# Optimization experiments

Measured on AMD Instinct MI355X. Metric: run time of the kernel, lower is better.

The kernel has to match this reference:

```python
import jax, jax.numpy as jnp
import numpy as np

RMS_EPS = 1.1920928955078125e-07  # torch.finfo(float32).eps, nn.RMSNorm default when eps=None


def setup_inputs() -> dict:
    key = jax.random.key(0)
    ks = jax.random.split(key, 7)
    B, T, C, Wh, E, K = 8, 4096, 256, 1024, 8, 2
    return {
        "x": jax.random.normal(ks[0], (B, T, C), dtype=jnp.float32),
        "rms_weight": jnp.ones((C,), dtype=jnp.float32),
        "W1": jax.random.normal(ks[1], (E, C, Wh), dtype=jnp.float32),
        "b1": jax.random.normal(ks[2], (E, Wh), dtype=jnp.float32),
        "W2": jax.random.normal(ks[3], (E, Wh, C), dtype=jnp.float32),
        "b2": jax.random.normal(ks[4], (E, C), dtype=jnp.float32),
        "expert_ids": jax.random.randint(ks[5], (B, T, K), 0, E, dtype=jnp.int64),
    }


def reference(x, rms_weight, W1, b1, W2, b2, expert_ids):
    # RMSNorm over last dim (torch nn.RMSNorm, eps = float32 eps)
    xn = x * jax.lax.rsqrt(jnp.mean(x * x, axis=-1, keepdims=True) + RMS_EPS) * rms_weight
    # Per-expert 2-layer MLP. The torch code gathers per-token weight copies then bmm's;
    # mathematically identical (and far cheaper in memory) is: run every expert densely,
    # then gather the K selected expert outputs per token.
    h = jax.nn.gelu(jnp.einsum("btc,ecw->btew", xn, W1) + b1, approximate=False)  # [B,T,E,Wh]
    y = jnp.einsum("btew,ewc->btec", h, W2) + b2  # [B,T,E,C]
    # gather selected experts: [B,T,K,C]; dropout p is 0.0 (eval) -> identity
    out = jnp.take_along_axis(y, expert_ids[..., None], axis=2)
    return out
```

## Files before the change

kernel.cpp:

```cpp
#include <hip/hip_runtime.h>
#include <cstdint>

typedef unsigned short ushort_t;
typedef __bf16 bf16x8 __attribute__((ext_vector_type(8)));
typedef ushort_t u16x8 __attribute__((ext_vector_type(8)));
typedef float f32x4 __attribute__((ext_vector_type(4)));
typedef uint32_t u32x4 __attribute__((ext_vector_type(4)));

#define RMS_EPS 1.1920928955078125e-07f

__device__ __forceinline__ ushort_t f2bf(float f) {
  uint32_t u = __builtin_bit_cast(uint32_t, f);
  u += 0x7fffu + ((u >> 16) & 1u);
  return (ushort_t)(u >> 16);
}

__device__ __forceinline__ void g2l16(const ushort_t* g, ushort_t* l) {
  __builtin_amdgcn_global_load_lds(
      (const __attribute__((address_space(1))) uint32_t*)g,
      (__attribute__((address_space(3))) uint32_t*)l, 16, 0, 0);
}

__global__ void rmsnorm_cast(const float* __restrict__ x, const float* __restrict__ w,
                             ushort_t* __restrict__ xn) {
  int token = blockIdx.x * 4 + (threadIdx.x >> 6);
  int lane = threadIdx.x & 63;
  const float4* row = reinterpret_cast<const float4*>(x + (size_t)token * 256);
  float4 v = row[lane];
  float s = v.x * v.x + v.y * v.y + v.z * v.z + v.w * v.w;
#pragma unroll
  for (int off = 1; off < 64; off <<= 1) s += __shfl_xor(s, off);
  float inv = rsqrtf(s * (1.0f / 256.0f) + RMS_EPS);
  const float4* wr = reinterpret_cast<const float4*>(w);
  float4 wv = wr[lane];
  ushort4 o;
  o.x = f2bf(v.x * inv * wv.x);
  o.y = f2bf(v.y * inv * wv.y);
  o.z = f2bf(v.z * inv * wv.z);
  o.w = f2bf(v.w * inv * wv.w);
  *reinterpret_cast<ushort4*>(xn + (size_t)token * 256 + lane * 4) = o;
}

__global__ __launch_bounds__(256) void pack_w(const float* __restrict__ W1,
                                              const float* __restrict__ W2,
                                              ushort_t* __restrict__ w1f,
                                              ushort_t* __restrict__ w2f) {
  __shared__ ushort_t tile[64][130];
  int b = blockIdx.x;
  int isW2 = b >= 256;
  const float* src; ushort_t* dst; int e, kt, wt, rs;
  if (!isW2) { e = b >> 5; kt = (b >> 3) & 3; wt = b & 7; src = W1; dst = w1f; rs = 1024; }
  else { b -= 256; e = b >> 5; kt = (b >> 1) & 15; wt = b & 1; src = W2; dst = w2f; rs = 256; }
  int k0 = kt * 64, c0 = wt * 128;
  const float* sb = src + ((size_t)e << 18) + (size_t)k0 * rs + c0;
  int t = threadIdx.x;
#pragma unroll
  for (int i = 0; i < 8; ++i) {
    int f = i * 1024 + t * 4;
    int r = f >> 7, c = f & 127;
    float4 v = *reinterpret_cast<const float4*>(sb + (size_t)r * rs + c);
    ushort2 lo, hi;
    lo.x = f2bf(v.x); lo.y = f2bf(v.y); hi.x = f2bf(v.z); hi.y = f2bf(v.w);
    *reinterpret_cast<ushort2*>(&tile[r][c]) = lo;
    *reinterpret_cast<ushort2*>(&tile[r][c + 2]) = hi;
  }
  __syncthreads();
  int lane = t & 63, l16 = lane & 15, quad = lane >> 4;
#pragma unroll
  for (int p = 0; p < 4; ++p) {
    int u = p * 256 + t;
    int kk2 = (u >> 9) & 1;
    int rr = kk2 * 32 + quad * 8;
    u16x8 o;
    size_t U;
    if (!isW2) {
      int nt = (u >> 6) & 1, chL = (u >> 7) & 3;
      int cc = chL * 32 + nt * 16 + l16;
#pragma unroll
      for (int j = 0; j < 8; ++j) o[j] = tile[rr + j][cc];
      U = ((size_t)e * 32768) + (size_t)(wt * 4 + chL) * 1024 + (kt * 2 + kk2) * 128 + nt * 64 + lane;
    } else {
      int ntL = (u >> 6) & 7;
      int cc = ntL * 16 + l16;
#pragma unroll
      for (int j = 0; j < 8; ++j) o[j] = tile[rr + j][cc];
      U = ((size_t)e * 32768) + (size_t)(kt * 2 + kk2) * 1024 + (wt * 8 + ntL) * 64 + lane;
    }
    *reinterpret_cast<u16x8*>(dst + U * 8) = o;
  }
}

__global__ void route_pairs(const int* __restrict__ eids, int* __restrict__ cnt,
                            int* __restrict__ lists) {
  __shared__ int lcnt[8], lbase[8];
  int tid = threadIdx.x;
  if (tid < 8) lcnt[tid] = 0;
  __syncthreads();
  int p = blockIdx.x * 256 + tid;
  int e = eids[p];
  int lpos = atomicAdd(&lcnt[e], 1);
  __syncthreads();
  if (tid < 8) lbase[tid] = atomicAdd(&cnt[tid], lcnt[tid]);
  __syncthreads();
  lists[e * 65536 + lbase[e] + lpos] = p;
}

__global__ __launch_bounds__(256, 2) void moe_mlp(
    const ushort_t* __restrict__ xn,
    const ushort_t* __restrict__ w1f,
    const ushort_t* __restrict__ w2f,
    const float* __restrict__ b1,
    const float* __restrict__ b2,
    const int* __restrict__ cnt,
    const int* __restrict__ lists,
    float* __restrict__ out)
{
  __shared__ __align__(16) ushort_t w1b[2][8192];
  __shared__ __align__(16) ushort_t w2b[2][8192];
  __shared__ __align__(16) ushort_t hlds[4][32][40];
  __shared__ int prs[128];

  int flat = blockIdx.x;
  int e = -1, tile = 0, accum = 0, n_e = 0;
#pragma unroll
  for (int i = 0; i < 8; ++i) {
    int c = cnt[i];
    int t = (c + 127) >> 7;
    if (e < 0 && flat < accum + t) { e = i; tile = flat - accum; n_e = c; }
    accum += t;
  }
  if (e < 0) return;
  int start = tile * 128;

  int tid = threadIdx.x;
  if (tid < 128) {
    int idx = start + tid;
    prs[tid] = (idx < n_e) ? lists[e * 65536 + idx] : lists[e * 65536];
  }

  const ushort_t* w1e = w1f + ((size_t)e << 18);
  const ushort_t* w2e = w2f + ((size_t)e << 18);
  int wave = tid >> 6, lane = tid & 63, l16 = lane & 15, quad = lane >> 4;

#pragma unroll
  for (int j = 0; j < 4; ++j) {
    int p = j * 4 + wave;
    g2l16(w1e + p * 512 + lane * 8, &w1b[0][p * 512]);
    g2l16(w2e + p * 512 + lane * 8, &w2b[0][p * 512]);
  }
  __syncthreads();

  bf16x8 afr[2][8];
#pragma unroll
  for (int mt = 0; mt < 2; ++mt) {
    int tok = prs[wave * 32 + mt * 16 + l16] >> 1;
    const u32x4* arow = reinterpret_cast<const u32x4*>(xn + (size_t)tok * 256);
#pragma unroll
    for (int kk = 0; kk < 8; ++kk)
      afr[mt][kk] = __builtin_bit_cast(bf16x8, arow[kk * 4 + quad]);
  }

  f32x4 acc[2][16];
#pragma unroll
  for (int mt = 0; mt < 2; ++mt)
#pragma unroll
    for (int ct = 0; ct < 16; ++ct) acc[mt][ct] = (f32x4){0.f, 0.f, 0.f, 0.f};

  const float* b1e = b1 + e * 1024;
  ushort_t* hl = &hlds[wave][0][0];

  for (int ch = 0; ch < 32; ++ch) {
    int cur = ch & 1;
    __syncthreads();
    if (ch + 1 < 32) {
      const ushort_t* n1 = w1e + (ch + 1) * 8192;
      const ushort_t* n2 = w2e + (ch + 1) * 8192;
#pragma unroll
      for (int j = 0; j < 4; ++j) {
        int p = j * 4 + wave;
        g2l16(n1 + p * 512 + lane * 8, &w1b[cur ^ 1][p * 512]);
        g2l16(n2 + p * 512 + lane * 8, &w2b[cur ^ 1][p * 512]);
      }
    }
    const ushort_t* l1 = w1b[cur];
    const ushort_t* l2 = w2b[cur];
    int w0 = ch * 32;
    float bias0 = b1e[w0 + l16];
    float bias1 = b1e[w0 + 16 + l16];

    f32x4 h00 = (f32x4){0.f, 0.f, 0.f, 0.f};
    f32x4 h01 = (f32x4){0.f, 0.f, 0.f, 0.f};
    f32x4 h10 = (f32x4){0.f, 0.f, 0.f, 0.f};
    f32x4 h11 = (f32x4){0.f, 0.f, 0.f, 0.f};
#pragma unroll
    for (int kk = 0; kk < 8; ++kk) {
      bf16x8 bA = *reinterpret_cast<const bf16x8*>(l1 + ((kk * 2 + 0) * 64 + lane) * 8);
      h00 = __builtin_amdgcn_mfma_f32_16x16x32_bf16(afr[0][kk], bA, h00, 0, 0, 0);
      h01 = __builtin_amdgcn_mfma_f32_16x16x32_bf16(afr[1][kk], bA, h01, 0, 0, 0);
    }
#pragma unroll
    for (int kk = 0; kk < 8; ++kk) {
      bf16x8 bB = *reinterpret_cast<const bf16x8*>(l1 + ((kk * 2 + 1) * 64 + lane) * 8);
      h10 = __builtin_amdgcn_mfma_f32_16x16x32_bf16(afr[0][kk], bB, h10, 0, 0, 0);
      h11 = __builtin_amdgcn_mfma_f32_16x16x32_bf16(afr[1][kk], bB, h11, 0, 0, 0);
    }
#pragma unroll
    for (int r = 0; r < 4; ++r) {
      {
        float v = h00[r] + bias0;
        float v2 = v * v;
        float u_ = (0.044715f * v2) * v + v;
        float tq = __expf(-1.5957691216057308f * u_);
        float g = v * __builtin_amdgcn_rcpf(1.0f + tq);
        hl[(quad * 4 + r) * 40 + l16] = f2bf(g);
      }
      {
        float v = h01[r] + bias0;
        float v2 = v * v;
        float u_ = (0.044715f * v2) * v + v;
        float tq = __expf(-1.5957691216057308f * u_);
        float g = v * __builtin_amdgcn_rcpf(1.0f + tq);
        hl[(16 + quad * 4 + r) * 40 + l16] = f2bf(g);
      }
      {
        float v = h10[r] + bias1;
        float v2 = v * v;
        float u_ = (0.044715f * v2) * v + v;
        float tq = __expf(-1.5957691216057308f * u_);
        float g = v * __builtin_amdgcn_rcpf(1.0f + tq);
        hl[(quad * 4 + r) * 40 + 16 + l16] = f2bf(g);
      }
      {
        float v = h11[r] + bias1;
        float v2 = v * v;
        float u_ = (0.044715f * v2) * v + v;
        float tq = __expf(-1.5957691216057308f * u_);
        float g = v * __builtin_amdgcn_rcpf(1.0f + tq);
        hl[(16 + quad * 4 + r) * 40 + 16 + l16] = f2bf(g);
      }
    }
    bf16x8 a2_0 = *reinterpret_cast<const bf16x8*>(hl + l16 * 40 + quad * 8);
    bf16x8 a2_1 = *reinterpret_cast<const bf16x8*>(hl + (16 + l16) * 40 + quad * 8);

#pragma unroll
    for (int ct = 0; ct < 16; ++ct) {
      bf16x8 b = *reinterpret_cast<const bf16x8*>(l2 + (ct * 64 + lane) * 8);
      acc[0][ct] = __builtin_amdgcn_mfma_f32_16x16x32_bf16(a2_0, b, acc[0][ct], 0, 0, 0);
      acc[1][ct] = __builtin_amdgcn_mfma_f32_16x16x32_bf16(a2_1, b, acc[1][ct], 0, 0, 0);
    }
  }

  const float* b2e = b2 + e * 256;
  float bl[16];
#pragma unroll
  for (int ct = 0; ct < 16; ++ct) bl[ct] = b2e[ct * 16 + l16];
#pragma unroll
  for (int mt = 0; mt < 2; ++mt) {
#pragma unroll
    for (int r = 0; r < 4; ++r) {
      int m = wave * 32 + mt * 16 + quad * 4 + r;
      if (start + m < n_e) {
        float* orow = out + (size_t)prs[m] * 256;
#pragma unroll
        for (int ct = 0; ct < 16; ++ct)
          orow[ct * 16 + l16] = acc[mt][ct][r] + bl[ct];
      }
    }
  }
}

extern "C" void kernel_launch(void* const* d_in, const int* in_sizes, int n_in,
                              void* d_out, int out_size, void* d_ws, size_t ws_size,
                              hipStream_t stream) {
  const float* x  = (const float*)d_in[0];
  const float* rw = (const float*)d_in[1];
  const float* W1 = (const float*)d_in[2];
  const float* b1 = (const float*)d_in[3];
  const float* W2 = (const float*)d_in[4];
  const float* b2 = (const float*)d_in[5];
  const int* eids = (const int*)d_in[6];
  float* out = (float*)d_out;

  char* ws = (char*)d_ws;
  ushort_t* xn  = (ushort_t*)(ws);
  ushort_t* w1f = (ushort_t*)(ws + 16777216);
  ushort_t* w2f = (ushort_t*)(ws + 20971520);
  int* cnt      = (int*)(ws + 25165824);
  int* lists    = (int*)(ws + 25166080);

  hipMemsetAsync(cnt, 0, 8 * sizeof(int), stream);
  rmsnorm_cast<<<8192, 256, 0, stream>>>(x, rw, xn);
  pack_w<<<512, 256, 0, stream>>>(W1, W2, w1f, w2f);
  route_pairs<<<256, 256, 0, stream>>>(eids, cnt, lists);
  moe_mlp<<<519, 256, 0, stream>>>(xn, w1f, w2f, b1, b2, cnt, lists, out);
}
```

Measured before the change: 253.3 us.

## Compute transposed MFMA products to keep GELU hidden in registers, dropping LDS round-trip

Both GEMMs now swap operands so each lane holds a token's column of results. GELU outputs can then be packed directly into the next MFMA's B operand, with no LDS staging of the hidden activations. The W2 prepack layout is changed to match. The W2 buffer is single-buffered, and a second barrier per chunk is added before the W2 MFMAs. Output stores become float4 vectors, and the token-index shared array is replaced with per-lane register loads. The trade-off is less overlap on W2 loads and an extra sync per chunk.

```diff
diff --git a/kernel.cpp b/kernel.cpp
--- a/kernel.cpp
+++ b/kernel.cpp
@@ -19,6 +19,17 @@
   __builtin_amdgcn_global_load_lds(
       (const __attribute__((address_space(1))) uint32_t*)g,
       (__attribute__((address_space(3))) uint32_t*)l, 16, 0, 0);
+}
+
+__device__ __forceinline__ f32x4 mfma32(bf16x8 a, bf16x8 b, f32x4 c) {
+  return __builtin_amdgcn_mfma_f32_16x16x32_bf16(a, b, c, 0, 0, 0);
+}
+
+__device__ __forceinline__ float gelu1(float v) {
+  float v2 = v * v;
+  float u_ = (0.044715f * v2) * v + v;
+  float tq = __expf(-1.5957691216057308f * u_);
+  return v * __builtin_amdgcn_rcpf(1.0f + tq);
 }
 
 __global__ void rmsnorm_cast(const float* __restrict__ x, const float* __restrict__ w,
@@ -66,27 +77,35 @@
   }
   __syncthreads();
   int lane = t & 63, l16 = lane & 15, quad = lane >> 4;
-#pragma unroll
-  for (int p = 0; p < 4; ++p) {
-    int u = p * 256 + t;
-    int kk2 = (u >> 9) & 1;
-    int rr = kk2 * 32 + quad * 8;
-    u16x8 o;
-    size_t U;
-    if (!isW2) {
+  int wave = t >> 6;
+  if (!isW2) {
+#pragma unroll
+    for (int p = 0; p < 4; ++p) {
+      int u = p * 256 + t;
+      int kk2 = (u >> 9) & 1;
+      int rr = kk2 * 32 + quad * 8;
       int nt = (u >> 6) & 1, chL = (u >> 7) & 3;
       int cc = chL * 32 + nt * 16 + l16;
+      u16x8 o;
 #pragma unroll
       for (int j = 0; j < 8; ++j) o[j] = tile[rr + j][cc];
-      U = ((size_t)e * 32768) + (size_t)(wt * 4 + chL) * 1024 + (kt * 2 + kk2) * 128 + nt * 64 + lane;
-    } else {
-      int ntL = (u >> 6) & 7;
-      int cc = ntL * 16 + l16;
-#pragma unroll
-      for (int j = 0; j < 8; ++j) o[j] = tile[rr + j][cc];
-      U = ((size_t)e * 32768) + (size_t)(kt * 2 + kk2) * 1024 + (wt * 8 + ntL) * 64 + lane;
-    }
-    *reinterpret_cast<u16x8*>(dst + U * 8) = o;
+      size_t U = ((size_t)e * 32768) + (size_t)(wt * 4 + chL) * 1024 + (kt * 2 + kk2) * 128 + nt * 64 + lane;
+      *reinterpret_cast<u16x8*>(dst + U * 8) = o;
+    }
+  } else {
+#pragma unroll
+    for (int p = 0; p < 4; ++p) {
+      int u = p * 4 + wave;
+      int chL = u >> 3, ctL = u & 7;
+      int cc = ctL * 16 + l16;
+      u16x8 o;
+#pragma unroll
+      for (int j = 0; j < 4; ++j) o[j] = tile[chL * 32 + quad * 4 + j][cc];
+#pragma unroll
+      for (int j = 0; j < 4; ++j) o[4 + j] = tile[chL * 32 + 16 + quad * 4 + j][cc];
+      size_t U = (((size_t)(e * 32 + kt * 2 + chL) * 16) + (wt * 8 + ctL)) * 64 + lane;
+      *reinterpret_cast<u16x8*>(dst + U * 8) = o;
+    }
   }
 }
 
@@ -116,9 +135,7 @@
     float* __restrict__ out)
 {
   __shared__ __align__(16) ushort_t w1b[2][8192];
-  __shared__ __align__(16) ushort_t w2b[2][8192];
-  __shared__ __align__(16) ushort_t hlds[4][32][40];
-  __shared__ int prs[128];
+  __shared__ __align__(16) ushort_t w2b[8192];
 
   int flat = blockIdx.x;
   int e = -1, tile = 0, accum = 0, n_e = 0;
@@ -133,31 +150,32 @@
   int start = tile * 128;
 
   int tid = threadIdx.x;
-  if (tid < 128) {
-    int idx = start + tid;
-    prs[tid] = (idx < n_e) ? lists[e * 65536 + idx] : lists[e * 65536];
-  }
+  int wave = tid >> 6, lane = tid & 63, l16 = lane & 15, quad = lane >> 4;
 
   const ushort_t* w1e = w1f + ((size_t)e << 18);
   const ushort_t* w2e = w2f + ((size_t)e << 18);
-  int wave = tid >> 6, lane = tid & 63, l16 = lane & 15, quad = lane >> 4;
+  const int* le = lists + e * 65536;
+
+  int gi0 = start + wave * 32 + l16;
+  int gi1 = gi0 + 16;
+  int pr0 = le[(gi0 < n_e) ? gi0 : 0];
+  int pr1 = le[(gi1 < n_e) ? gi1 : 0];
 
 #pragma unroll
   for (int j = 0; j < 4; ++j) {
     int p = j * 4 + wave;
     g2l16(w1e + p * 512 + lane * 8, &w1b[0][p * 512]);
-    g2l16(w2e + p * 512 + lane * 8, &w2b[0][p * 512]);
-  }
-  __syncthreads();
+  }
 
   bf16x8 afr[2][8];
-#pragma unroll
-  for (int mt = 0; mt < 2; ++mt) {
-    int tok = prs[wave * 32 + mt * 16 + l16] >> 1;
-    const u32x4* arow = reinterpret_cast<const u32x4*>(xn + (size_t)tok * 256);
-#pragma unroll
-    for (int kk = 0; kk < 8; ++kk)
-      afr[mt][kk] = __builtin_bit_cast(bf16x8, arow[kk * 4 + quad]);
+  {
+    const u32x4* ar0 = reinterpret_cast<const u32x4*>(xn + (size_t)(pr0 >> 1) * 256);
+    const u32x4* ar1 = reinterpret_cast<const u32x4*>(xn + (size_t)(pr1 >> 1) * 256);
+#pragma unroll
+    for (int kk = 0; kk < 8; ++kk) {
+      afr[0][kk] = __builtin_bit_cast(bf16x8, ar0[kk * 4 + quad]);
+      afr[1][kk] = __builtin_bit_cast(bf16x8, ar1[kk * 4 + quad]);
+    }
   }
 
   f32x4 acc[2][16];
@@ -167,103 +185,80 @@
     for (int ct = 0; ct < 16; ++ct) acc[mt][ct] = (f32x4){0.f, 0.f, 0.f, 0.f};
 
   const float* b1e = b1 + e * 1024;
-  ushort_t* hl = &hlds[wave][0][0];
 
   for (int ch = 0; ch < 32; ++ch) {
     int cur = ch & 1;
     __syncthreads();
+
+    {
+      const ushort_t* n2 = w2e + ch * 8192;
+#pragma unroll
+      for (int j = 0; j < 4; ++j) {
+        int p = j * 4 + wave;
+        g2l16(n2 + p * 512 + lane * 8, &w2b[p * 512]);
+      }
+    }
     if (ch + 1 < 32) {
       const ushort_t* n1 = w1e + (ch + 1) * 8192;
-      const ushort_t* n2 = w2e + (ch + 1) * 8192;
 #pragma unroll
       for (int j = 0; j < 4; ++j) {
         int p = j * 4 + wave;
         g2l16(n1 + p * 512 + lane * 8, &w1b[cur ^ 1][p * 512]);
-        g2l16(n2 + p * 512 + lane * 8, &w2b[cur ^ 1][p * 512]);
       }
     }
+
+    int w0 = ch * 32;
+    f32x4 bia0 = *reinterpret_cast<const f32x4*>(b1e + w0 + quad * 4);
+    f32x4 bia1 = *reinterpret_cast<const f32x4*>(b1e + w0 + 16 + quad * 4);
+
     const ushort_t* l1 = w1b[cur];
-    const ushort_t* l2 = w2b[cur];
-    int w0 = ch * 32;
-    float bias0 = b1e[w0 + l16];
-    float bias1 = b1e[w0 + 16 + l16];
-
-    f32x4 h00 = (f32x4){0.f, 0.f, 0.f, 0.f};
-    f32x4 h01 = (f32x4){0.f, 0.f, 0.f, 0.f};
-    f32x4 h10 = (f32x4){0.f, 0.f, 0.f, 0.f};
-    f32x4 h11 = (f32x4){0.f, 0.f, 0.f, 0.f};
+    f32x4 ht00 = (f32x4){0.f, 0.f, 0.f, 0.f};
+    f32x4 ht01 = (f32x4){0.f, 0.f, 0.f, 0.f};
+    f32x4 ht10 = (f32x4){0.f, 0.f, 0.f, 0.f};
+    f32x4 ht11 = (f32x4){0.f, 0.f, 0.f, 0.f};
 #pragma unroll
     for (int kk = 0; kk < 8; ++kk) {
-      bf16x8 bA = *reinterpret_cast<const bf16x8*>(l1 + ((kk * 2 + 0) * 64 + lane) * 8);
-      h00 = __builtin_amdgcn_mfma_f32_16x16x32_bf16(afr[0][kk], bA, h00, 0, 0, 0);
-      h01 = __builtin_amdgcn_mfma_f32_16x16x32_bf16(afr[1][kk], bA, h01, 0, 0, 0);
-    }
-#pragma unroll
-    for (int kk = 0; kk < 8; ++kk) {
-      bf16x8 bB = *reinterpret_cast<const bf16x8*>(l1 + ((kk * 2 + 1) * 64 + lane) * 8);
-      h10 = __builtin_amdgcn_mfma_f32_16x16x32_bf16(afr[0][kk], bB, h10, 0, 0, 0);
-      h11 = __builtin_amdgcn_mfma_f32_16x16x32_bf16(afr[1][kk], bB, h11, 0, 0, 0);
-    }
+      bf16x8 wA = *reinterpret_cast<const bf16x8*>(l1 + ((kk * 2 + 0) * 64 + lane) * 8);
+      bf16x8 wB = *reinterpret_cast<const bf16x8*>(l1 + ((kk * 2 + 1) * 64 + lane) * 8);
+      ht00 = mfma32(wA, afr[0][kk], ht00);
+      ht10 = mfma32(wA, afr[1][kk], ht10);
+      ht01 = mfma32(wB, afr[0][kk], ht01);
+      ht11 = mfma32(wB, afr[1][kk], ht11);
+    }
+
+    u16x8 hp0, hp1;
 #pragma unroll
     for (int r = 0; r < 4; ++r) {
-      {
-        float v = h00[r] + bias0;
-        float v2 = v * v;
-        float u_ = (0.044715f * v2) * v + v;
-        float tq = __expf(-1.5957691216057308f * u_);
-        float g = v * __builtin_amdgcn_rcpf(1.0f + tq);
-        hl[(quad * 4 + r) * 40 + l16] = f2bf(g);
-      }
-      {
-        float v = h01[r] + bias0;
-        float v2 = v * v;
-        float u_ = (0.044715f * v2) * v + v;
-        float tq = __expf(-1.5957691216057308f * u_);
-        float g = v * __builtin_amdgcn_rcpf(1.0f + tq);
-        hl[(16 + quad * 4 + r) * 40 + l16] = f2bf(g);
-      }
-      {
-        float v = h10[r] + bias1;
-        float v2 = v * v;
-        float u_ = (0.044715f * v2) * v + v;
-        float tq = __expf(-1.5957691216057308f * u_);
-        float g = v * __builtin_amdgcn_rcpf(1.0f + tq);
-        hl[(quad * 4 + r) * 40 + 16 + l16] = f2bf(g);
-      }
-      {
-        float v = h11[r] + bias1;
-        float v2 = v * v;
-        float u_ = (0.044715f * v2) * v + v;
-        float tq = __expf(-1.5957691216057308f * u_);
-        float g = v * __builtin_amdgcn_rcpf(1.0f + tq);
-        hl[(16 + quad * 4 + r) * 40 + 16 + l16] = f2bf(g);
-      }
-    }
-    bf16x8 a2_0 = *reinterpret_cast<const bf16x8*>(hl + l16 * 40 + quad * 8);
-    bf16x8 a2_1 = *reinterpret_cast<const bf16x8*>(hl + (16 + l16) * 40 + quad * 8);
+      hp0[r]     = f2bf(gelu1(ht00[r] + bia0[r]));
+      hp0[4 + r] = f2bf(gelu1(ht01[r] + bia1[r]));
+      hp1[r]     = f2bf(gelu1(ht10[r] + bia0[r]));
+      hp1[4 + r] = f2bf(gelu1(ht11[r] + bia1[r]));
+    }
+    bf16x8 hF0 = __builtin_bit_cast(bf16x8, hp0);
+    bf16x8 hF1 = __builtin_bit_cast(bf16x8, hp1);
+
+    __syncthreads();
 
 #pragma unroll
     for (int ct = 0; ct < 16; ++ct) {
-      bf16x8 b = *reinterpret_cast<const bf16x8*>(l2 + (ct * 64 + lane) * 8);
-      acc[0][ct] = __builtin_amdgcn_mfma_f32_16x16x32_bf16(a2_0, b, acc[0][ct], 0, 0, 0);
-      acc[1][ct] = __builtin_amdgcn_mfma_f32_16x16x32_bf16(a2_1, b, acc[1][ct], 0, 0, 0);
+      bf16x8 wq = *reinterpret_cast<const bf16x8*>(w2b + (ct * 64 + lane) * 8);
+      acc[0][ct] = mfma32(wq, hF0, acc[0][ct]);
+      acc[1][ct] = mfma32(wq, hF1, acc[1][ct]);
     }
   }
 
   const float* b2e = b2 + e * 256;
-  float bl[16];
-#pragma unroll
-  for (int ct = 0; ct < 16; ++ct) bl[ct] = b2e[ct * 16 + l16];
 #pragma unroll
   for (int mt = 0; mt < 2; ++mt) {
-#pragma unroll
-    for (int r = 0; r < 4; ++r) {
-      int m = wave * 32 + mt * 16 + quad * 4 + r;
-      if (start + m < n_e) {
-        float* orow = out + (size_t)prs[m] * 256;
-#pragma unroll
-        for (int ct = 0; ct < 16; ++ct)
-          orow[ct * 16 + l16] = acc[mt][ct][r] + bl[ct];
+    int gi = mt ? gi1 : gi0;
+    int pr = mt ? pr1 : pr0;
+    if (gi < n_e) {
+      float* orow = out + (size_t)pr * 256;
+#pragma unroll
+      for (int ct = 0; ct < 16; ++ct) {
+        f32x4 bv = *reinterpret_cast<const f32x4*>(b2e + ct * 16 + quad * 4);
+        f32x4 o = acc[mt][ct] + bv;
+        *reinterpret_cast<f32x4*>(orow + ct * 16 + quad * 4) = o;
       }
     }
   }
```

Result: slower. 259.9 us (+2.6%).
